# Performance work log

Measured on AMD Instinct MI355X. Metric: run time of the kernel, lower is better.

## Reference

```python
import jax, jax.numpy as jnp
import numpy as np

NUM_USER = 100000
NUM_ENT = 200000
NUM_REL = 32
DIM = 64
N_NEIGHBOR = 16
BATCH = 16384


def setup_inputs() -> dict:
    key = jax.random.key(0)
    ks = jax.random.split(key, 11)
    inp = {
        "u": jax.random.randint(ks[0], (BATCH,), 0, NUM_USER),
        "v": jax.random.randint(ks[1], (BATCH,), 0, NUM_ENT),
        "user_neighbor": jax.random.randint(ks[2], (BATCH, N_NEIGHBOR), 0, NUM_ENT),
        "item_neighbor": jax.random.randint(ks[3], (BATCH, N_NEIGHBOR), 0, NUM_USER),
        "adj_ent": jax.random.randint(ks[4], (NUM_ENT, N_NEIGHBOR), 0, NUM_ENT),
        "adj_rel": jax.random.randint(ks[5], (NUM_ENT, N_NEIGHBOR), 0, NUM_REL),
        "usr_emb": jax.random.normal(ks[6], (NUM_USER, DIM), dtype=jnp.float32) * 0.1,
        "ent_emb": jax.random.normal(ks[7], (NUM_ENT, DIM), dtype=jnp.float32) * 0.1,
        "rel_emb": jax.random.normal(ks[8], (NUM_REL, DIM), dtype=jnp.float32) * 0.1,
        "agg_W": jax.random.normal(ks[9], (DIM, DIM), dtype=jnp.float32) * (1.0 / np.sqrt(DIM)),
        "agg_b": jax.random.normal(ks[10], (DIM,), dtype=jnp.float32) * 0.01,
    }
    return inp


def reference(u, v, user_neighbor, item_neighbor, adj_ent, adj_rel,
              usr_emb, ent_emb, rel_emb, agg_W, agg_b):
    n = N_NEIGHBOR
    # LightGCN-style "lite" embeddings: mean over sampled interaction neighbors
    lite_user = usr_emb[item_neighbor].sum(axis=1) * (1.0 / n)   # [B, D]
    lite_item = ent_emb[user_neighbor].sum(axis=1) * (1.0 / n)   # [B, D]

    user_embeddings = usr_emb[u]                                  # [B, D]
    item_embeddings_original = ent_emb[v]                         # [B, D]

    # one-hop KG neighbors of items
    nbr_ent = adj_ent[v]                                          # [B, n]
    nbr_rel = adj_rel[v]                                          # [B, n]
    self_vectors = item_embeddings_original[:, None, :]           # [B, 1, D]
    neighbor_vectors = ent_emb[nbr_ent][:, None, :, :]            # [B, 1, n, D]
    neighbor_relations = rel_emb[nbr_rel][:, None, :, :]          # [B, 1, n, D]

    # KGCN sum-aggregator: user-relation attention over neighbors
    ur_scores = jnp.einsum("bd,bknd->bkn", user_embeddings, neighbor_relations)
    attn = jax.nn.softmax(ur_scores, axis=-1)                     # [B, 1, n]
    neighbors_agg = jnp.einsum("bkn,bknd->bkd", attn, neighbor_vectors)
    combined = self_vectors + neighbors_agg                       # [B, 1, D]
    item_embeddings = jnp.tanh(combined @ agg_W + agg_b)[:, 0, :]  # [B, D]

    user_final = 0.5 * lite_user + 0.5 * user_embeddings
    item_final = 0.5 * lite_item + 0.5 * item_embeddings
    scores = jnp.sum(user_final * item_final, axis=1)
    return jax.nn.sigmoid(scores)
```

## Files before the change

### kernel.cpp

```cpp
#include <hip/hip_runtime.h>
#include <math.h>

#define DIM 64
#define NNB 16
#define BATCH 16384

template <int WPB>
__global__ __launch_bounds__(WPB * 64, 2) void klgcn_kernel(
    const int* __restrict__ u, const int* __restrict__ v,
    const int* __restrict__ user_neighbor, const int* __restrict__ item_neighbor,
    const int* __restrict__ adj_ent, const int* __restrict__ adj_rel,
    const float* __restrict__ usr_emb, const float* __restrict__ ent_emb,
    const float* __restrict__ rel_emb, const float* __restrict__ agg_W,
    const float* __restrict__ agg_b, float* __restrict__ out)
{
    const int wave = threadIdx.x >> 6;
    const int lane = threadIdx.x & 63;
    int b = blockIdx.x * WPB + wave;
    b = __builtin_amdgcn_readfirstlane(b);

    __shared__ float comb_lds[WPB][DIM];

    const int ub = __builtin_amdgcn_readfirstlane(u[b]);
    const int vb = __builtin_amdgcn_readfirstlane(v[b]);

    const float ue = usr_emb[(long)ub * DIM + lane];
    const float ie = ent_emb[(long)vb * DIM + lane];

    int i_it[NNB], i_un[NNB], i_ar[NNB], i_ae[NNB];
#pragma unroll
    for (int n = 0; n < NNB; n++)
        i_it[n] = __builtin_amdgcn_readfirstlane(item_neighbor[b * NNB + n]);
#pragma unroll
    for (int n = 0; n < NNB; n++)
        i_un[n] = __builtin_amdgcn_readfirstlane(user_neighbor[b * NNB + n]);
#pragma unroll
    for (int n = 0; n < NNB; n++)
        i_ar[n] = __builtin_amdgcn_readfirstlane(adj_rel[vb * NNB + n]);
#pragma unroll
    for (int n = 0; n < NNB; n++)
        i_ae[n] = __builtin_amdgcn_readfirstlane(adj_ent[vb * NNB + n]);

    float r_lu[NNB], r_li[NNB], r_re[NNB], r_ag[NNB];
#pragma unroll
    for (int n = 0; n < NNB; n++) r_lu[n] = usr_emb[(long)i_it[n] * DIM + lane];
#pragma unroll
    for (int n = 0; n < NNB; n++) r_li[n] = ent_emb[(long)i_un[n] * DIM + lane];
#pragma unroll
    for (int n = 0; n < NNB; n++) r_re[n] = rel_emb[i_ar[n] * DIM + lane];
#pragma unroll
    for (int n = 0; n < NNB; n++) r_ag[n] = ent_emb[(long)i_ae[n] * DIM + lane];

    float lite_user = 0.f;
#pragma unroll
    for (int n = 0; n < NNB; n++) lite_user += r_lu[n];
    lite_user *= (1.0f / NNB);

    float lite_item = 0.f;
#pragma unroll
    for (int n = 0; n < NNB; n++) lite_item += r_li[n];
    lite_item *= (1.0f / NNB);

    float attn[NNB];
#pragma unroll
    for (int n = 0; n < NNB; n++) {
        float p = ue * r_re[n];
#pragma unroll
        for (int s = 32; s > 0; s >>= 1) p += __shfl_xor(p, s, 64);
        attn[n] = p;
    }

    float m = attn[0];
#pragma unroll
    for (int n = 1; n < NNB; n++) m = fmaxf(m, attn[n]);
    float ssum = 0.f;
#pragma unroll
    for (int n = 0; n < NNB; n++) {
        attn[n] = __expf(attn[n] - m);
        ssum += attn[n];
    }
    const float inv = 1.0f / ssum;

    float agg = 0.f;
#pragma unroll
    for (int n = 0; n < NNB; n++) agg += attn[n] * r_ag[n];
    agg *= inv;

    const float combined = ie + agg;
    comb_lds[wave][lane] = combined;

    float acc = agg_b[lane];
#pragma unroll
    for (int d = 0; d < DIM; d++) {
        acc = fmaf(comb_lds[wave][d], agg_W[d * DIM + lane], acc);
    }
    const float item_emb = tanhf(acc);

    const float uf = 0.5f * (lite_user + ue);
    const float itf = 0.5f * (lite_item + item_emb);

    float p = uf * itf;
#pragma unroll
    for (int s = 32; s > 0; s >>= 1) p += __shfl_xor(p, s, 64);

    if (lane == 0) out[b] = 1.0f / (1.0f + __expf(-p));
}

extern "C" void kernel_launch(void* const* d_in, const int* in_sizes, int n_in,
                              void* d_out, int out_size, void* d_ws, size_t ws_size,
                              hipStream_t stream)
{
    const int*   u             = (const int*)d_in[0];
    const int*   v             = (const int*)d_in[1];
    const int*   user_neighbor = (const int*)d_in[2];
    const int*   item_neighbor = (const int*)d_in[3];
    const int*   adj_ent       = (const int*)d_in[4];
    const int*   adj_rel       = (const int*)d_in[5];
    const float* usr_emb       = (const float*)d_in[6];
    const float* ent_emb       = (const float*)d_in[7];
    const float* rel_emb       = (const float*)d_in[8];
    const float* agg_W         = (const float*)d_in[9];
    const float* agg_b         = (const float*)d_in[10];
    float* out = (float*)d_out;

    constexpr int WPB = 4;
    dim3 grid(BATCH / WPB), block(WPB * 64);
    klgcn_kernel<WPB><<<grid, block, 0, stream>>>(
        u, v, user_neighbor, item_neighbor, adj_ent, adj_rel,
        usr_emb, ent_emb, rel_emb, agg_W, agg_b, out);
}
```

Baseline: 151.2 us.

## Restructure wave into 4 groups of 16 lanes with float4 row gathers

Each wave is split into four 16-lane groups. Each lane loads a float4 slice of an embedding row, so one row is fetched by 16 lanes and four neighbors are handled at once. Attention scores, the softmax and the aggregations use reductions within and across groups. The LDS-staged matvec becomes a shuffle-broadcast matvec that reads W as float4 and reduces across groups. Launch bounds are raised to 4 blocks per CU, which trades register budget for occupancy and adds shuffle overhead.

```diff
diff --git a/kernel.cpp b/kernel.cpp
--- a/kernel.cpp
+++ b/kernel.cpp
@@ -5,8 +5,22 @@
 #define NNB 16
 #define BATCH 16384
 
+typedef float4 f4;
+
+__device__ __forceinline__ float dot4(const f4 a, const f4 b) {
+    return fmaf(a.x, b.x, fmaf(a.y, b.y, fmaf(a.z, b.z, a.w * b.w)));
+}
+
+__device__ __forceinline__ f4 xgrp_sum(f4 v) {
+    v.x += __shfl_xor(v.x, 16, 64); v.y += __shfl_xor(v.y, 16, 64);
+    v.z += __shfl_xor(v.z, 16, 64); v.w += __shfl_xor(v.w, 16, 64);
+    v.x += __shfl_xor(v.x, 32, 64); v.y += __shfl_xor(v.y, 32, 64);
+    v.z += __shfl_xor(v.z, 32, 64); v.w += __shfl_xor(v.w, 32, 64);
+    return v;
+}
+
 template <int WPB>
-__global__ __launch_bounds__(WPB * 64, 2) void klgcn_kernel(
+__global__ __launch_bounds__(WPB * 64, 4) void klgcn_kernel(
     const int* __restrict__ u, const int* __restrict__ v,
     const int* __restrict__ user_neighbor, const int* __restrict__ item_neighbor,
     const int* __restrict__ adj_ent, const int* __restrict__ adj_rel,
@@ -16,16 +30,18 @@
 {
     const int wave = threadIdx.x >> 6;
     const int lane = threadIdx.x & 63;
-    int b = blockIdx.x * WPB + wave;
-    b = __builtin_amdgcn_readfirstlane(b);
+    const int g = lane >> 4;
+    const int s = lane & 15;
+    const int b = __builtin_amdgcn_readfirstlane(blockIdx.x * WPB + wave);
 
-    __shared__ float comb_lds[WPB][DIM];
+    const f4* __restrict__ usr4 = (const f4*)usr_emb;
+    const f4* __restrict__ ent4 = (const f4*)ent_emb;
+    const f4* __restrict__ rel4 = (const f4*)rel_emb;
+    const f4* __restrict__ W4   = (const f4*)agg_W;
+    const f4* __restrict__ b4p  = (const f4*)agg_b;
 
     const int ub = __builtin_amdgcn_readfirstlane(u[b]);
     const int vb = __builtin_amdgcn_readfirstlane(v[b]);
-
-    const float ue = usr_emb[(long)ub * DIM + lane];
-    const float ie = ent_emb[(long)vb * DIM + lane];
 
     int i_it[NNB], i_un[NNB], i_ar[NNB], i_ae[NNB];
 #pragma unroll
@@ -41,67 +57,99 @@
     for (int n = 0; n < NNB; n++)
         i_ae[n] = __builtin_amdgcn_readfirstlane(adj_ent[vb * NNB + n]);
 
-    float r_lu[NNB], r_li[NNB], r_re[NNB], r_ag[NNB];
+    f4 ue4 = usr4[(long)ub * 16 + s];
+    f4 ie4 = ent4[(long)vb * 16 + s];
+    f4 Re[4], Ag[4], Lu[4], Li[4];
 #pragma unroll
-    for (int n = 0; n < NNB; n++) r_lu[n] = usr_emb[(long)i_it[n] * DIM + lane];
+    for (int k = 0; k < 4; k++) Re[k] = rel4[i_ar[4 * k + g] * 16 + s];
 #pragma unroll
-    for (int n = 0; n < NNB; n++) r_li[n] = ent_emb[(long)i_un[n] * DIM + lane];
+    for (int k = 0; k < 4; k++) Ag[k] = ent4[(long)i_ae[4 * k + g] * 16 + s];
 #pragma unroll
-    for (int n = 0; n < NNB; n++) r_re[n] = rel_emb[i_ar[n] * DIM + lane];
+    for (int k = 0; k < 4; k++) Lu[k] = usr4[(long)i_it[4 * k + g] * 16 + s];
 #pragma unroll
-    for (int n = 0; n < NNB; n++) r_ag[n] = ent_emb[(long)i_ae[n] * DIM + lane];
+    for (int k = 0; k < 4; k++) Li[k] = ent4[(long)i_un[4 * k + g] * 16 + s];
 
-    float lite_user = 0.f;
+    float sc[4];
 #pragma unroll
-    for (int n = 0; n < NNB; n++) lite_user += r_lu[n];
-    lite_user *= (1.0f / NNB);
-
-    float lite_item = 0.f;
-#pragma unroll
-    for (int n = 0; n < NNB; n++) lite_item += r_li[n];
-    lite_item *= (1.0f / NNB);
-
-    float attn[NNB];
-#pragma unroll
-    for (int n = 0; n < NNB; n++) {
-        float p = ue * r_re[n];
-#pragma unroll
-        for (int s = 32; s > 0; s >>= 1) p += __shfl_xor(p, s, 64);
-        attn[n] = p;
+    for (int k = 0; k < 4; k++) {
+        float p = dot4(ue4, Re[k]);
+        p += __shfl_xor(p, 1, 64); p += __shfl_xor(p, 2, 64);
+        p += __shfl_xor(p, 4, 64); p += __shfl_xor(p, 8, 64);
+        sc[k] = p;
     }
-
-    float m = attn[0];
-#pragma unroll
-    for (int n = 1; n < NNB; n++) m = fmaxf(m, attn[n]);
+    float m = fmaxf(fmaxf(sc[0], sc[1]), fmaxf(sc[2], sc[3]));
+    m = fmaxf(m, __shfl_xor(m, 16, 64));
+    m = fmaxf(m, __shfl_xor(m, 32, 64));
+    float e[4];
     float ssum = 0.f;
 #pragma unroll
-    for (int n = 0; n < NNB; n++) {
-        attn[n] = __expf(attn[n] - m);
-        ssum += attn[n];
-    }
+    for (int k = 0; k < 4; k++) { e[k] = __expf(sc[k] - m); ssum += e[k]; }
+    ssum += __shfl_xor(ssum, 16, 64);
+    ssum += __shfl_xor(ssum, 32, 64);
     const float inv = 1.0f / ssum;
 
-    float agg = 0.f;
+    f4 ag = {0.f, 0.f, 0.f, 0.f};
 #pragma unroll
-    for (int n = 0; n < NNB; n++) agg += attn[n] * r_ag[n];
-    agg *= inv;
+    for (int k = 0; k < 4; k++) {
+        ag.x = fmaf(e[k], Ag[k].x, ag.x);
+        ag.y = fmaf(e[k], Ag[k].y, ag.y);
+        ag.z = fmaf(e[k], Ag[k].z, ag.z);
+        ag.w = fmaf(e[k], Ag[k].w, ag.w);
+    }
+    ag = xgrp_sum(ag);
 
-    const float combined = ie + agg;
-    comb_lds[wave][lane] = combined;
+    f4 comb;
+    comb.x = fmaf(ag.x, inv, ie4.x);
+    comb.y = fmaf(ag.y, inv, ie4.y);
+    comb.z = fmaf(ag.z, inv, ie4.z);
+    comb.w = fmaf(ag.w, inv, ie4.w);
+    const float cc[4] = {comb.x, comb.y, comb.z, comb.w};
 
-    float acc = agg_b[lane];
+    f4 lu;
+    lu.x = Lu[0].x + Lu[1].x + Lu[2].x + Lu[3].x;
+    lu.y = Lu[0].y + Lu[1].y + Lu[2].y + Lu[3].y;
+    lu.z = Lu[0].z + Lu[1].z + Lu[2].z + Lu[3].z;
+    lu.w = Lu[0].w + Lu[1].w + Lu[2].w + Lu[3].w;
+    lu = xgrp_sum(lu);
+    f4 li;
+    li.x = Li[0].x + Li[1].x + Li[2].x + Li[3].x;
+    li.y = Li[0].y + Li[1].y + Li[2].y + Li[3].y;
+    li.z = Li[0].z + Li[1].z + Li[2].z + Li[3].z;
+    li.w = Li[0].w + Li[1].w + Li[2].w + Li[3].w;
+    li = xgrp_sum(li);
+
+    f4 acc = {0.f, 0.f, 0.f, 0.f};
 #pragma unroll
-    for (int d = 0; d < DIM; d++) {
-        acc = fmaf(comb_lds[wave][d], agg_W[d * DIM + lane], acc);
+    for (int j = 0; j < 16; j++) {
+        const int d = 16 * g + j;
+        const float cd = __shfl(cc[j & 3], 20 * g + (j >> 2), 64);
+        const f4 w = W4[d * 16 + s];
+        acc.x = fmaf(cd, w.x, acc.x);
+        acc.y = fmaf(cd, w.y, acc.y);
+        acc.z = fmaf(cd, w.z, acc.z);
+        acc.w = fmaf(cd, w.w, acc.w);
     }
-    const float item_emb = tanhf(acc);
+    acc = xgrp_sum(acc);
+    const f4 bias = b4p[s];
+    f4 item4;
+    item4.x = tanhf(acc.x + bias.x);
+    item4.y = tanhf(acc.y + bias.y);
+    item4.z = tanhf(acc.z + bias.z);
+    item4.w = tanhf(acc.w + bias.w);
 
-    const float uf = 0.5f * (lite_user + ue);
-    const float itf = 0.5f * (lite_item + item_emb);
+    f4 uf, itf;
+    uf.x = 0.5f * fmaf(lu.x, 1.f / NNB, ue4.x);
+    uf.y = 0.5f * fmaf(lu.y, 1.f / NNB, ue4.y);
+    uf.z = 0.5f * fmaf(lu.z, 1.f / NNB, ue4.z);
+    uf.w = 0.5f * fmaf(lu.w, 1.f / NNB, ue4.w);
+    itf.x = 0.5f * fmaf(li.x, 1.f / NNB, item4.x);
+    itf.y = 0.5f * fmaf(li.y, 1.f / NNB, item4.y);
+    itf.z = 0.5f * fmaf(li.z, 1.f / NNB, item4.z);
+    itf.w = 0.5f * fmaf(li.w, 1.f / NNB, item4.w);
 
-    float p = uf * itf;
-#pragma unroll
-    for (int s = 32; s > 0; s >>= 1) p += __shfl_xor(p, s, 64);
+    float p = dot4(uf, itf);
+    p += __shfl_xor(p, 1, 64); p += __shfl_xor(p, 2, 64);
+    p += __shfl_xor(p, 4, 64); p += __shfl_xor(p, 8, 64);
 
     if (lane == 0) out[b] = 1.0f / (1.0f + __expf(-p));
 }
```

Result: slower. 178.1 us (+17.8%).
